# Kernel tuning notes

Hardware: AMD Instinct MI355X
Metric: run time of the kernel (lower is better)

The kernel has to match this reference:

```python
import jax, jax.numpy as jnp
import numpy as np

RADIUS = 0.1
K = 32  # num_neighbors


def _ball_query(points, centers, radius, k):
    # points: [B,3,N], centers: [B,3,M] -> indices [B,M,K] (int32)
    # PVCNN semantics: first k point indices within radius of each center,
    # unfilled slots padded with the first in-ball index (0 if none in ball).
    N = points.shape[-1]
    p2 = jnp.sum(points * points, axis=1)            # [B,N]
    c2 = jnp.sum(centers * centers, axis=1)          # [B,M]
    cp = jnp.einsum('bdm,bdn->bmn', centers, points)  # [B,M,N]
    dist2 = c2[:, :, None] + p2[:, None, :] - 2.0 * cp
    valid = dist2 < radius * radius                  # [B,M,N]
    # score = point index if in ball else sentinel N; sorting ascending puts
    # the first k in-ball indices (in original point order) up front.
    scores = jnp.where(valid, jnp.arange(N, dtype=jnp.int32), jnp.int32(N))
    idx = jnp.sort(scores, axis=-1)[..., :k]         # [B,M,K]
    first = idx[..., :1]
    first = jnp.where(first == N, 0, first)          # no neighbor -> index 0
    return jnp.where(idx == N, first, idx)


def _group(feat, idx):
    # feat: [B,C,N], idx: [B,M,K] -> [B,C,M,K]
    return jnp.take_along_axis(feat[:, :, None, :], idx[:, None, :, :], axis=3)


def setup_inputs() -> dict:
    key = jax.random.key(0)
    k1, k2, k3 = jax.random.split(key, 3)
    B, N, M, C = 2, 16384, 4096, 32
    points_coords = jax.random.uniform(k1, (B, 3, N), dtype=jnp.float32)
    centers_coords = jax.random.uniform(k2, (B, 3, M), dtype=jnp.float32)
    points_features = jax.random.normal(k3, (B, C, N), dtype=jnp.float32)
    return {
        'points_coords': points_coords,
        'centers_coords': centers_coords,
        'points_features': points_features,
    }


def reference(points_coords, centers_coords, points_features):
    idx = _ball_query(points_coords, centers_coords, RADIUS, K)     # [B,M,K]
    nbr_coords = _group(points_coords, idx)                          # [B,3,M,K]
    nbr_coords = nbr_coords - centers_coords[:, :, :, None]         # relative
    nbr_feats = _group(points_features, idx)                         # [B,C,M,K]
    out = jnp.concatenate([nbr_coords, nbr_feats], axis=1)          # [B,3+C,M,K]
    return jnp.transpose(out, (0, 1, 3, 2))                          # [B,3+C,K,M]
```

## Files before the change

### kernel.cpp

```cpp
#include <hip/hip_runtime.h>

#define B_SZ  2
#define N_PTS 16384
#define M_CTR 4096
#define C_FT  32
#define K_NB  32
#define NCH   35
#define CH_STRIDE (K_NB * M_CTR)
#define CELLS 10
#define NCELL (CELLS * CELLS * CELLS)

__device__ __forceinline__ float fmul(float a, float b) {
    float r; asm("v_mul_f32 %0, %1, %2" : "=v"(r) : "v"(a), "v"(b)); return r;
}
__device__ __forceinline__ float fadd(float a, float b) {
    float r; asm("v_add_f32 %0, %1, %2" : "=v"(r) : "v"(a), "v"(b)); return r;
}
__device__ __forceinline__ float fsub(float a, float b) {
    float r; asm("v_sub_f32 %0, %1, %2" : "=v"(r) : "v"(a), "v"(b)); return r;
}
__device__ __forceinline__ float ffma(float a, float b, float c) {
    float r; asm("v_fma_f32 %0, %1, %2, %3" : "=v"(r) : "v"(a), "v"(b), "v"(c));
    return r;
}

__device__ __forceinline__ bool bq_valid(float x, float y, float z,
                                         float cx, float cy, float cz,
                                         float c2, float r2) {
    const float p2 = fadd(fadd(fmul(x, x), fmul(y, y)), fmul(z, z));
    const float cp = ffma(cz, z, ffma(cy, y, fmul(cx, x)));
    return fsub(fadd(c2, p2), fmul(2.0f, cp)) < r2;
}

__device__ __forceinline__ int cell_of(float x, float y, float z) {
    int ci = (int)(x * 10.0f); ci = ci < 0 ? 0 : (ci > 9 ? 9 : ci);
    int cj = (int)(y * 10.0f); cj = cj < 0 ? 0 : (cj > 9 ? 9 : cj);
    int ck = (int)(z * 10.0f); ck = ck < 0 ? 0 : (ck > 9 ? 9 : ck);
    return (ck * CELLS + cj) * CELLS + ci;
}

__global__ __launch_bounds__(256) void hist_kernel(
    const float* __restrict__ points, int* __restrict__ hist) {
    const int t = blockIdx.x * 256 + threadIdx.x;
    const int b = t >> 14, n = t & (N_PTS - 1);
    const float x = points[(b * 3 + 0) * N_PTS + n];
    const float y = points[(b * 3 + 1) * N_PTS + n];
    const float z = points[(b * 3 + 2) * N_PTS + n];
    atomicAdd(&hist[b * NCELL + cell_of(x, y, z)], 1);
}

__global__ __launch_bounds__(1024) void scan_kernel(
    const int* __restrict__ hist, int* __restrict__ starts,
    int* __restrict__ cursor) {
    const int b = blockIdx.x;
    const int t = threadIdx.x;
    const int lane = t & 63, wid = t >> 6;
    __shared__ int wsum[16];
    const int v = (t < NCELL) ? hist[b * NCELL + t] : 0;
    int incl = v;
    for (int off = 1; off < 64; off <<= 1) {
        const int u = __shfl_up(incl, off);
        if (lane >= off) incl += u;
    }
    if (lane == 63) wsum[wid] = incl;
    __syncthreads();
    if (wid == 0 && lane < 16) {
        const int s = wsum[lane];
        int in2 = s;
        for (int off = 1; off < 16; off <<= 1) {
            const int u = __shfl_up(in2, off);
            if (lane >= off) in2 += u;
        }
        wsum[lane] = in2 - s;
    }
    __syncthreads();
    if (t < NCELL) {
        const int excl = incl - v + wsum[wid];
        starts[b * (NCELL + 1) + t] = excl;
        cursor[b * NCELL + t] = excl;
        if (t == NCELL - 1) starts[b * (NCELL + 1) + NCELL] = excl + v;
    }
}

__global__ __launch_bounds__(256) void scatter_transpose_kernel(
    const float* __restrict__ points, const float* __restrict__ feats,
    int* __restrict__ cursor, float4* __restrict__ binned,
    float* __restrict__ pf) {
    if (blockIdx.x < 128) {
        const int t = blockIdx.x * 256 + threadIdx.x;
        const int b = t >> 14, n = t & (N_PTS - 1);
        const float x = points[(b * 3 + 0) * N_PTS + n];
        const float y = points[(b * 3 + 1) * N_PTS + n];
        const float z = points[(b * 3 + 2) * N_PTS + n];
        const int pos = atomicAdd(&cursor[b * NCELL + cell_of(x, y, z)], 1);
        binned[b * N_PTS + pos] = make_float4(x, y, z, __int_as_float(n));
    } else {
        __shared__ float tile[64][37];
        const int bid = blockIdx.x - 128;
        const int t  = threadIdx.x;
        const int b  = bid >> 8;
        const int n0 = (bid & 255) * 64;
        for (int i = t; i < NCH * 64; i += 256) {
            const int r = i >> 6;
            const int c = i & 63;
            float v;
            if (r < 3) v = points[(b * 3 + r) * N_PTS + n0 + c];
            else       v = feats[(b * C_FT + (r - 3)) * N_PTS + n0 + c];
            tile[c][r] = v;
        }
        if (t < 64) tile[t][35] = 0.0f;
        __syncthreads();
        float* __restrict__ dst = pf + ((size_t)b * N_PTS + n0) * 36;
        for (int o = t; o < 64 * 36; o += 256) {
            const int c = o / 36;
            const int r = o - c * 36;
            dst[o] = tile[c][r];
        }
    }
}

__global__ __launch_bounds__(256) void ball_query_kernel(
    const float4* __restrict__ binned,
    const float* __restrict__ centers,
    const int* __restrict__ starts,
    int* __restrict__ idx_out)
{
    const int lane = threadIdx.x & 63;
    const int wid  = threadIdx.x >> 6;
    const int cid  = blockIdx.x * 4 + wid;
    const int b = cid >> 12;
    const int m = cid & (M_CTR - 1);

    const float r2 = (float)(0.1 * 0.1);

    const float cx = centers[(b * 3 + 0) * M_CTR + m];
    const float cy = centers[(b * 3 + 1) * M_CTR + m];
    const float cz = centers[(b * 3 + 2) * M_CTR + m];
    const float c2 = fadd(fadd(fmul(cx, cx), fmul(cy, cy)), fmul(cz, cz));

    __shared__ unsigned bitmap[4][N_PTS / 32];
    unsigned* bm = bitmap[wid];
#pragma unroll
    for (int j = 0; j < 8; ++j) bm[lane * 8 + j] = 0u;

    int ci = (int)(cx * 10.0f); ci = ci < 0 ? 0 : (ci > 9 ? 9 : ci);
    int cj = (int)(cy * 10.0f); cj = cj < 0 ? 0 : (cj > 9 ? 9 : cj);
    int ck = (int)(cz * 10.0f); ck = ck < 0 ? 0 : (ck > 9 ? 9 : ck);
    const int i0 = ci > 0 ? ci - 1 : 0;
    const int i1 = ci < 9 ? ci + 1 : 9;
    const int* st = starts + b * (NCELL + 1);
    const float4* __restrict__ bp = binned + b * N_PTS;

    for (int d = 0; d < 9; ++d) {
        const int jj = cj + (d % 3) - 1;
        const int kk = ck + (d / 3) - 1;
        if (jj < 0 || jj > 9 || kk < 0 || kk > 9) continue;
        const int base = (kk * CELLS + jj) * CELLS;
        const int lo = st[base + i0];
        const int hi = st[base + i1 + 1];
        for (int s0 = lo; s0 < hi; s0 += 64) {
            const int t = s0 + lane;
            if (t < hi) {
                const float4 p = bp[t];
                if (bq_valid(p.x, p.y, p.z, cx, cy, cz, c2, r2)) {
                    const int n = __float_as_int(p.w);
                    atomicOr((int*)&bm[n >> 5], 1 << (n & 31));
                }
            }
        }
    }

    unsigned w[8];
    int cnt = 0;
#pragma unroll
    for (int j = 0; j < 8; ++j) { w[j] = bm[lane * 8 + j]; cnt += __popc(w[j]); }

    int incl = cnt;
    for (int off = 1; off < 64; off <<= 1) {
        const int v = __shfl_up(incl, off);
        if (lane >= off) incl += v;
    }
    const int total = __shfl(incl, 63);
    int slot = incl - cnt;

    int firstbit = 0x7fffffff;
#pragma unroll
    for (int j = 0; j < 8; ++j) {
        if (w[j] && firstbit == 0x7fffffff)
            firstbit = lane * 256 + j * 32 + (__ffs(w[j]) - 1);
    }
    for (int off = 32; off > 0; off >>= 1)
        firstbit = min(firstbit, __shfl_xor(firstbit, off));
    const int first_idx = (total == 0) ? 0 : firstbit;

    int* __restrict__ dst = idx_out + (b * K_NB) * M_CTR + m;
#pragma unroll
    for (int j = 0; j < 8; ++j) {
        unsigned x = w[j];
        while (x && slot < K_NB) {
            const int bit = __ffs(x) - 1;
            dst[slot * M_CTR] = lane * 256 + j * 32 + bit;
            x &= x - 1;
            ++slot;
        }
    }
    if (lane >= total && lane < K_NB) dst[lane * M_CTR] = first_idx;
}

__global__ __launch_bounds__(256) void gather_kernel(
    const float* __restrict__ pf,
    const float* __restrict__ centers,
    const int* __restrict__ idx,
    float* __restrict__ out)
{
    const int t = blockIdx.x * 256 + threadIdx.x;
    const int m = (t & (M_CTR / 2 - 1)) * 2;
    const int k = (t >> 11) & (K_NB - 1);
    const int b = t >> 16;

    const int2 nn = *(const int2*)&idx[(b * K_NB + k) * M_CTR + m];
    const float4* __restrict__ s0 =
        (const float4*)(pf + ((size_t)b * N_PTS + nn.x) * 36);
    const float4* __restrict__ s1 =
        (const float4*)(pf + ((size_t)b * N_PTS + nn.y) * 36);

    float4 f0[9], f1[9];
#pragma unroll
    for (int i = 0; i < 9; ++i) { f0[i] = s0[i]; f1[i] = s1[i]; }

    const float2 cx = *(const float2*)&centers[(b * 3 + 0) * M_CTR + m];
    const float2 cy = *(const float2*)&centers[(b * 3 + 1) * M_CTR + m];
    const float2 cz = *(const float2*)&centers[(b * 3 + 2) * M_CTR + m];

    float v0[36], v1[36];
#pragma unroll
    for (int i = 0; i < 9; ++i) {
        v0[4 * i + 0] = f0[i].x; v0[4 * i + 1] = f0[i].y;
        v0[4 * i + 2] = f0[i].z; v0[4 * i + 3] = f0[i].w;
        v1[4 * i + 0] = f1[i].x; v1[4 * i + 1] = f1[i].y;
        v1[4 * i + 2] = f1[i].z; v1[4 * i + 3] = f1[i].w;
    }
    v0[0] -= cx.x; v0[1] -= cy.x; v0[2] -= cz.x;
    v1[0] -= cx.y; v1[1] -= cy.y; v1[2] -= cz.y;

    float* __restrict__ o = out + ((size_t)b * NCH * K_NB + k) * M_CTR + m;
#pragma unroll
    for (int ch = 0; ch < NCH; ++ch)
        *(float2*)&o[(size_t)ch * CH_STRIDE] = make_float2(v0[ch], v1[ch]);
}

extern "C" void kernel_launch(void* const* d_in, const int* in_sizes, int n_in,
                              void* d_out, int out_size, void* d_ws, size_t ws_size,
                              hipStream_t stream) {
    const float* points  = (const float*)d_in[0];
    const float* centers = (const float*)d_in[1];
    const float* feats   = (const float*)d_in[2];
    float* out = (float*)d_out;

    char* ws = (char*)d_ws;
    int*    idx    = (int*)ws;
    float*  pf     = (float*)(ws + (1u << 20));
    int*    hist   = (int*)(ws + 5700 * 1024);
    int*    cursor = (int*)(ws + 5716 * 1024);
    int*    starts = (int*)(ws + 5732 * 1024);
    float4* binned = (float4*)(ws + 5764 * 1024);

    hipMemsetAsync(hist, 0, B_SZ * NCELL * sizeof(int), stream);
    hist_kernel<<<(B_SZ * N_PTS) / 256, 256, 0, stream>>>(points, hist);
    scan_kernel<<<B_SZ, 1024, 0, stream>>>(hist, starts, cursor);
    scatter_transpose_kernel<<<128 + B_SZ * (N_PTS / 64), 256, 0, stream>>>(
        points, feats, cursor, binned, pf);
    ball_query_kernel<<<(B_SZ * M_CTR) / 4, 256, 0, stream>>>(
        binned, centers, starts, idx);
    gather_kernel<<<(B_SZ * K_NB * M_CTR / 2) / 256, 256, 0, stream>>>(
        pf, centers, idx, out);
}
```

Measured before the change: 108.6 us.

## Split gather across channel groups with four centers per thread

The gather kernel now gives each thread one 4-channel group of the 36-float point record for four consecutive centers, instead of all 36 channels for two centers. This raises the thread count ninefold, cuts per-thread registers, and widens stores to float4, so more memory requests can be in flight at once. In exchange, each neighbour index is reloaded by nine threads and gather reads become 16-byte pieces scattered across many threads.

```diff
diff --git a/kernel.cpp b/kernel.cpp
--- a/kernel.cpp
+++ b/kernel.cpp
@@ -214,39 +214,36 @@
     float* __restrict__ out)
 {
     const int t = blockIdx.x * 256 + threadIdx.x;
-    const int m = (t & (M_CTR / 2 - 1)) * 2;
-    const int k = (t >> 11) & (K_NB - 1);
-    const int b = t >> 16;
-
-    const int2 nn = *(const int2*)&idx[(b * K_NB + k) * M_CTR + m];
-    const float4* __restrict__ s0 =
-        (const float4*)(pf + ((size_t)b * N_PTS + nn.x) * 36);
-    const float4* __restrict__ s1 =
-        (const float4*)(pf + ((size_t)b * N_PTS + nn.y) * 36);
-
-    float4 f0[9], f1[9];
-#pragma unroll
-    for (int i = 0; i < 9; ++i) { f0[i] = s0[i]; f1[i] = s1[i]; }
-
-    const float2 cx = *(const float2*)&centers[(b * 3 + 0) * M_CTR + m];
-    const float2 cy = *(const float2*)&centers[(b * 3 + 1) * M_CTR + m];
-    const float2 cz = *(const float2*)&centers[(b * 3 + 2) * M_CTR + m];
-
-    float v0[36], v1[36];
-#pragma unroll
-    for (int i = 0; i < 9; ++i) {
-        v0[4 * i + 0] = f0[i].x; v0[4 * i + 1] = f0[i].y;
-        v0[4 * i + 2] = f0[i].z; v0[4 * i + 3] = f0[i].w;
-        v1[4 * i + 0] = f1[i].x; v1[4 * i + 1] = f1[i].y;
-        v1[4 * i + 2] = f1[i].z; v1[4 * i + 3] = f1[i].w;
-    }
-    v0[0] -= cx.x; v0[1] -= cy.x; v0[2] -= cz.x;
-    v1[0] -= cx.y; v1[1] -= cy.y; v1[2] -= cz.y;
-
-    float* __restrict__ o = out + ((size_t)b * NCH * K_NB + k) * M_CTR + m;
-#pragma unroll
-    for (int ch = 0; ch < NCH; ++ch)
-        *(float2*)&o[(size_t)ch * CH_STRIDE] = make_float2(v0[ch], v1[ch]);
+    const int g = t >> 16;
+    const int rem = t & 65535;
+    const int m = (rem & (M_CTR / 4 - 1)) * 4;
+    const int k = (rem >> 10) & (K_NB - 1);
+    const int b = rem >> 15;
+
+    const int4 nn = *(const int4*)&idx[(b * K_NB + k) * M_CTR + m];
+    const size_t pb = (size_t)b * N_PTS;
+    float4 a = *(const float4*)(pf + (pb + nn.x) * 36 + g * 4);
+    float4 e = *(const float4*)(pf + (pb + nn.y) * 36 + g * 4);
+    float4 f = *(const float4*)(pf + (pb + nn.z) * 36 + g * 4);
+    float4 h = *(const float4*)(pf + (pb + nn.w) * 36 + g * 4);
+
+    if (g == 0) {
+        const float4 cx = *(const float4*)&centers[(b * 3 + 0) * M_CTR + m];
+        const float4 cy = *(const float4*)&centers[(b * 3 + 1) * M_CTR + m];
+        const float4 cz = *(const float4*)&centers[(b * 3 + 2) * M_CTR + m];
+        a.x -= cx.x; a.y -= cy.x; a.z -= cz.x;
+        e.x -= cx.y; e.y -= cy.y; e.z -= cz.y;
+        f.x -= cx.z; f.y -= cy.z; f.z -= cz.z;
+        h.x -= cx.w; h.y -= cy.w; h.z -= cz.w;
+    }
+
+    float* __restrict__ o = out + ((size_t)b * NCH * K_NB + k) * M_CTR + m
+                          + (size_t)(4 * g) * CH_STRIDE;
+    *(float4*)&o[0]             = make_float4(a.x, e.x, f.x, h.x);
+    *(float4*)&o[CH_STRIDE]     = make_float4(a.y, e.y, f.y, h.y);
+    *(float4*)&o[2 * CH_STRIDE] = make_float4(a.z, e.z, f.z, h.z);
+    if (g < 8)
+        *(float4*)&o[3 * (size_t)CH_STRIDE] = make_float4(a.w, e.w, f.w, h.w);
 }
 
 extern "C" void kernel_launch(void* const* d_in, const int* in_sizes, int n_in,
@@ -272,6 +269,6 @@
         points, feats, cursor, binned, pf);
     ball_query_kernel<<<(B_SZ * M_CTR) / 4, 256, 0, stream>>>(
         binned, centers, starts, idx);
-    gather_kernel<<<(B_SZ * K_NB * M_CTR / 2) / 256, 256, 0, stream>>>(
+    gather_kernel<<<(9 * B_SZ * K_NB * (M_CTR / 4)) / 256, 256, 0, stream>>>(
         pf, centers, idx, out);
 }
```

Result: slower. 112.7 us (+3.8%).

## Fuse histogram and scan into one LDS-based prep kernel with the transpose

Applied to the files above, without the earlier changes.

Replaces the memset, global-atomic histogram kernel and scan kernel with a single prep kernel. Two blocks (one per batch) build the cell histogram in shared memory and scan it directly, and the remaining blocks of the same launch do the feature transpose. The point scatter moves into its own kernel. This removes a memset and a launch and swaps global atomics for LDS atomics. In exchange, the histogram for each batch now runs in only one block, and the transpose blocks are now 1024 threads wide, so most threads sit idle in the loops.

```diff
diff --git a/kernel.cpp b/kernel.cpp
--- a/kernel.cpp
+++ b/kernel.cpp
@@ -39,68 +39,63 @@
     return (ck * CELLS + cj) * CELLS + ci;
 }
 
-__global__ __launch_bounds__(256) void hist_kernel(
-    const float* __restrict__ points, int* __restrict__ hist) {
-    const int t = blockIdx.x * 256 + threadIdx.x;
-    const int b = t >> 14, n = t & (N_PTS - 1);
-    const float x = points[(b * 3 + 0) * N_PTS + n];
-    const float y = points[(b * 3 + 1) * N_PTS + n];
-    const float z = points[(b * 3 + 2) * N_PTS + n];
-    atomicAdd(&hist[b * NCELL + cell_of(x, y, z)], 1);
-}
-
-__global__ __launch_bounds__(1024) void scan_kernel(
-    const int* __restrict__ hist, int* __restrict__ starts,
-    int* __restrict__ cursor) {
-    const int b = blockIdx.x;
-    const int t = threadIdx.x;
-    const int lane = t & 63, wid = t >> 6;
-    __shared__ int wsum[16];
-    const int v = (t < NCELL) ? hist[b * NCELL + t] : 0;
-    int incl = v;
-    for (int off = 1; off < 64; off <<= 1) {
-        const int u = __shfl_up(incl, off);
-        if (lane >= off) incl += u;
-    }
-    if (lane == 63) wsum[wid] = incl;
-    __syncthreads();
-    if (wid == 0 && lane < 16) {
-        const int s = wsum[lane];
-        int in2 = s;
-        for (int off = 1; off < 16; off <<= 1) {
-            const int u = __shfl_up(in2, off);
-            if (lane >= off) in2 += u;
-        }
-        wsum[lane] = in2 - s;
-    }
-    __syncthreads();
-    if (t < NCELL) {
-        const int excl = incl - v + wsum[wid];
-        starts[b * (NCELL + 1) + t] = excl;
-        cursor[b * NCELL + t] = excl;
-        if (t == NCELL - 1) starts[b * (NCELL + 1) + NCELL] = excl + v;
-    }
-}
-
-__global__ __launch_bounds__(256) void scatter_transpose_kernel(
-    const float* __restrict__ points, const float* __restrict__ feats,
-    int* __restrict__ cursor, float4* __restrict__ binned,
-    float* __restrict__ pf) {
-    if (blockIdx.x < 128) {
-        const int t = blockIdx.x * 256 + threadIdx.x;
-        const int b = t >> 14, n = t & (N_PTS - 1);
-        const float x = points[(b * 3 + 0) * N_PTS + n];
-        const float y = points[(b * 3 + 1) * N_PTS + n];
-        const float z = points[(b * 3 + 2) * N_PTS + n];
-        const int pos = atomicAdd(&cursor[b * NCELL + cell_of(x, y, z)], 1);
-        binned[b * N_PTS + pos] = make_float4(x, y, z, __int_as_float(n));
+__global__ __launch_bounds__(1024) void prep_kernel(
+    const float* __restrict__ points,
+    const float* __restrict__ feats,
+    int* __restrict__ starts,
+    int* __restrict__ cursor,
+    float* __restrict__ pf)
+{
+    if (blockIdx.x < B_SZ) {
+        const int b = blockIdx.x;
+        const int t = threadIdx.x;
+        const int lane = t & 63, wid = t >> 6;
+        __shared__ int h[NCELL];
+        __shared__ int wsum[16];
+        for (int c = t; c < NCELL; c += 1024) h[c] = 0;
+        __syncthreads();
+
+        const float* __restrict__ px = points + (b * 3 + 0) * N_PTS;
+        const float* __restrict__ py = points + (b * 3 + 1) * N_PTS;
+        const float* __restrict__ pz = points + (b * 3 + 2) * N_PTS;
+#pragma unroll
+        for (int i = 0; i < 16; ++i) {
+            const int n = t + i * 1024;
+            atomicAdd(&h[cell_of(px[n], py[n], pz[n])], 1);
+        }
+        __syncthreads();
+
+        const int v = (t < NCELL) ? h[t] : 0;
+        int incl = v;
+        for (int off = 1; off < 64; off <<= 1) {
+            const int u = __shfl_up(incl, off);
+            if (lane >= off) incl += u;
+        }
+        if (lane == 63) wsum[wid] = incl;
+        __syncthreads();
+        if (wid == 0 && lane < 16) {
+            const int s = wsum[lane];
+            int in2 = s;
+            for (int off = 1; off < 16; off <<= 1) {
+                const int u = __shfl_up(in2, off);
+                if (lane >= off) in2 += u;
+            }
+            wsum[lane] = in2 - s;
+        }
+        __syncthreads();
+        if (t < NCELL) {
+            const int excl = incl - v + wsum[wid];
+            starts[b * (NCELL + 1) + t] = excl;
+            cursor[b * NCELL + t] = excl;
+            if (t == NCELL - 1) starts[b * (NCELL + 1) + NCELL] = excl + v;
+        }
     } else {
         __shared__ float tile[64][37];
-        const int bid = blockIdx.x - 128;
+        const int bid = blockIdx.x - B_SZ;
         const int t  = threadIdx.x;
         const int b  = bid >> 8;
         const int n0 = (bid & 255) * 64;
-        for (int i = t; i < NCH * 64; i += 256) {
+        for (int i = t; i < NCH * 64; i += 1024) {
             const int r = i >> 6;
             const int c = i & 63;
             float v;
@@ -111,12 +106,24 @@
         if (t < 64) tile[t][35] = 0.0f;
         __syncthreads();
         float* __restrict__ dst = pf + ((size_t)b * N_PTS + n0) * 36;
-        for (int o = t; o < 64 * 36; o += 256) {
+        for (int o = t; o < 64 * 36; o += 1024) {
             const int c = o / 36;
             const int r = o - c * 36;
             dst[o] = tile[c][r];
         }
     }
+}
+
+__global__ __launch_bounds__(256) void scatter_kernel(
+    const float* __restrict__ points, int* __restrict__ cursor,
+    float4* __restrict__ binned) {
+    const int t = blockIdx.x * 256 + threadIdx.x;
+    const int b = t >> 14, n = t & (N_PTS - 1);
+    const float x = points[(b * 3 + 0) * N_PTS + n];
+    const float y = points[(b * 3 + 1) * N_PTS + n];
+    const float z = points[(b * 3 + 2) * N_PTS + n];
+    const int pos = atomicAdd(&cursor[b * NCELL + cell_of(x, y, z)], 1);
+    binned[b * N_PTS + pos] = make_float4(x, y, z, __int_as_float(n));
 }
 
 __global__ __launch_bounds__(256) void ball_query_kernel(
@@ -260,16 +267,14 @@
     char* ws = (char*)d_ws;
     int*    idx    = (int*)ws;
     float*  pf     = (float*)(ws + (1u << 20));
-    int*    hist   = (int*)(ws + 5700 * 1024);
     int*    cursor = (int*)(ws + 5716 * 1024);
     int*    starts = (int*)(ws + 5732 * 1024);
     float4* binned = (float4*)(ws + 5764 * 1024);
 
-    hipMemsetAsync(hist, 0, B_SZ * NCELL * sizeof(int), stream);
-    hist_kernel<<<(B_SZ * N_PTS) / 256, 256, 0, stream>>>(points, hist);
-    scan_kernel<<<B_SZ, 1024, 0, stream>>>(hist, starts, cursor);
-    scatter_transpose_kernel<<<128 + B_SZ * (N_PTS / 64), 256, 0, stream>>>(
-        points, feats, cursor, binned, pf);
+    prep_kernel<<<B_SZ + B_SZ * (N_PTS / 64), 1024, 0, stream>>>(
+        points, feats, starts, cursor, pf);
+    scatter_kernel<<<(B_SZ * N_PTS) / 256, 256, 0, stream>>>(
+        points, cursor, binned);
     ball_query_kernel<<<(B_SZ * M_CTR) / 4, 256, 0, stream>>>(
         binned, centers, starts, idx);
     gather_kernel<<<(B_SZ * K_NB * M_CTR / 2) / 256, 256, 0, stream>>>(
```

Result: faster. 103.9 us (-4.4%).
